# Kernel tuning notes

Hardware: AMD Instinct MI355X
Metric: run time of the kernel (lower is better)

Reference implementation:

```python
import jax, jax.numpy as jnp
import numpy as np

INPUT_SIZE = 300
HIDDEN_SIZE = 600
NUM_LAYERS = 2
B, T = 64, 512


def setup_inputs() -> dict:
    key = jax.random.key(0)
    ks = jax.random.split(key, 2 + 4 * NUM_LAYERS)
    scale = 1.0 / np.sqrt(HIDDEN_SIZE)
    inp = {
        "start_input": jax.random.normal(ks[0], (B, T, INPUT_SIZE), dtype=jnp.float32),
        "hidden_state": jax.random.normal(ks[1], (NUM_LAYERS, B, HIDDEN_SIZE), dtype=jnp.float32),
    }
    for l in range(NUM_LAYERS):
        in_dim = INPUT_SIZE if l == 0 else HIDDEN_SIZE
        k0, k1, k2, k3 = ks[2 + 4 * l: 6 + 4 * l]
        inp[f"W_ih{l}"] = jax.random.uniform(k0, (3 * HIDDEN_SIZE, in_dim), minval=-scale, maxval=scale, dtype=jnp.float32)
        inp[f"W_hh{l}"] = jax.random.uniform(k1, (3 * HIDDEN_SIZE, HIDDEN_SIZE), minval=-scale, maxval=scale, dtype=jnp.float32)
        inp[f"b_ih{l}"] = jax.random.uniform(k2, (3 * HIDDEN_SIZE,), minval=-scale, maxval=scale, dtype=jnp.float32)
        inp[f"b_hh{l}"] = jax.random.uniform(k3, (3 * HIDDEN_SIZE,), minval=-scale, maxval=scale, dtype=jnp.float32)
    return inp


def _gru_layer(x, h0, W_ih, W_hh, b_ih, b_hh):
    # x: [B,T,D], h0: [B,H]. PyTorch GRU gate order: r, z, n.
    H = HIDDEN_SIZE
    gi_all = jnp.einsum("btd,gd->btg", x, W_ih) + b_ih  # [B,T,3H], input-side GEMM batched over time

    def step(h, gi):
        gh = h @ W_hh.T + b_hh  # [B,3H]
        r = jax.nn.sigmoid(gi[:, :H] + gh[:, :H])
        z = jax.nn.sigmoid(gi[:, H:2 * H] + gh[:, H:2 * H])
        n = jnp.tanh(gi[:, 2 * H:] + r * gh[:, 2 * H:])
        h_new = (1.0 - z) * n + z * h
        return h_new, h_new

    h_last, out = jax.lax.scan(step, h0, jnp.swapaxes(gi_all, 0, 1))  # scan over T
    return jnp.swapaxes(out, 0, 1), h_last  # [B,T,H], [B,H]


def reference(start_input, hidden_state, W_ih0, W_hh0, b_ih0, b_hh0, W_ih1, W_hh1, b_ih1, b_hh1):
    params = [(W_ih0, W_hh0, b_ih0, b_hh0), (W_ih1, W_hh1, b_ih1, b_hh1)]
    x = start_input
    h_finals = []
    for l in range(NUM_LAYERS):
        x, h_last = _gru_layer(x, hidden_state[l], *params[l])
        h_finals.append(h_last)
    # judge=True path: restack of per-timestep slices is identity on r_out
    ret = x
    hidden_out = jnp.stack(h_finals, axis=0)  # [num_layers, B, H]
    return ret, hidden_out
```

## Files before the change

### kernel.cpp

```cpp
#include <hip/hip_runtime.h>

#define B    64
#define T    512
#define H    600
#define G3   1800
#define IN0  300
#define NBLK 150
#define NTHR 256
#define KPAD 1208

#define WC0_OFF 0
#define WC0_SZ  (900 * G3)
#define WC1_OFF (WC0_OFF + WC0_SZ)
#define WC1_SZ  (1200 * G3)
#define BC0_OFF (WC1_OFF + WC1_SZ)
#define BC1_OFF (BC0_OFF + H * 4)
#define HA_OFF  (BC1_OFF + H * 4)
#define HB_OFF  (HA_OFF + B * H)
#define BAR_OFF (HB_OFF + B * H + 64)

__device__ __forceinline__ void grid_barrier(int* __restrict__ cnt, int* __restrict__ gen) {
    __syncthreads();
    if (threadIdx.x == 0) {
        int g = __hip_atomic_load(gen, __ATOMIC_RELAXED, __HIP_MEMORY_SCOPE_AGENT);
        int arrived = __hip_atomic_fetch_add(cnt, 1, __ATOMIC_ACQ_REL, __HIP_MEMORY_SCOPE_AGENT);
        if (arrived == NBLK - 1) {
            __hip_atomic_store(cnt, 0, __ATOMIC_RELAXED, __HIP_MEMORY_SCOPE_AGENT);
            __hip_atomic_fetch_add(gen, 1, __ATOMIC_ACQ_REL, __HIP_MEMORY_SCOPE_AGENT);
        } else {
            while (__hip_atomic_load(gen, __ATOMIC_ACQUIRE, __HIP_MEMORY_SCOPE_AGENT) == g) {
                __builtin_amdgcn_s_sleep(1);
            }
        }
    }
    __syncthreads();
}

__global__ void init_bar(int* bar) { bar[0] = 0; bar[32] = 0; }

__global__ void build_wc(const float* __restrict__ Wih, const float* __restrict__ Whh,
                         float* __restrict__ WC, int in_dim, int ktot) {
    int idx = blockIdx.x * blockDim.x + threadIdx.x;
    if (idx >= ktot * G3) return;
    int k = idx / G3;
    int c = idx - k * G3;
    int j = c / 3;
    int g = c - j * 3;
    int grow = g * H + j;
    float v = (k < in_dim) ? Wih[grow * in_dim + k] : Whh[grow * H + (k - in_dim)];
    WC[idx] = v;
}

__global__ void build_bc(const float* __restrict__ bih0, const float* __restrict__ bhh0,
                         const float* __restrict__ bih1, const float* __restrict__ bhh1,
                         float* __restrict__ BC0, float* __restrict__ BC1) {
    int j = blockIdx.x * blockDim.x + threadIdx.x;
    if (j >= H) return;
    BC0[j * 4 + 0] = bih0[j] + bhh0[j];
    BC0[j * 4 + 1] = bih0[H + j] + bhh0[H + j];
    BC0[j * 4 + 2] = bih0[2 * H + j];
    BC0[j * 4 + 3] = bhh0[2 * H + j];
    BC1[j * 4 + 0] = bih1[j] + bhh1[j];
    BC1[j * 4 + 1] = bih1[H + j] + bhh1[H + j];
    BC1[j * 4 + 2] = bih1[2 * H + j];
    BC1[j * 4 + 3] = bhh1[2 * H + j];
}

template<int N4, int CH>
__device__ __forceinline__ void dot3f(const float4* __restrict__ ap,
                                      const float* __restrict__ wr,
                                      const float* __restrict__ wz,
                                      const float* __restrict__ wn,
                                      float& sr, float& sz, float& sn) {
    constexpr int NCH = N4 / CH;
    static_assert(N4 % CH == 0, "chunking");
    float4 A[CH], Bf[CH];
    #pragma unroll
    for (int i = 0; i < CH; ++i) A[i] = ap[i];
    #pragma unroll 1
    for (int c = 0; c < NCH; c += 2) {
        if (c + 1 < NCH) {
            const float4* p = ap + (c + 1) * CH;
            #pragma unroll
            for (int i = 0; i < CH; ++i) Bf[i] = p[i];
        }
        #pragma unroll
        for (int i = 0; i < CH; ++i) {
            const int k = (c * CH + i) * 4;
            float4 a = A[i];
            const float4 wR = *(const float4*)(wr + k);
            const float4 wZ = *(const float4*)(wz + k);
            const float4 wN = *(const float4*)(wn + k);
            sr += a.x * wR.x + a.y * wR.y + a.z * wR.z + a.w * wR.w;
            sz += a.x * wZ.x + a.y * wZ.y + a.z * wZ.z + a.w * wZ.w;
            sn += a.x * wN.x + a.y * wN.y + a.z * wN.z + a.w * wN.w;
        }
        if (c + 1 < NCH) {
            if (c + 2 < NCH) {
                const float4* p = ap + (c + 2) * CH;
                #pragma unroll
                for (int i = 0; i < CH; ++i) A[i] = p[i];
            }
            #pragma unroll
            for (int i = 0; i < CH; ++i) {
                const int k = ((c + 1) * CH + i) * 4;
                float4 a = Bf[i];
                const float4 wR = *(const float4*)(wr + k);
                const float4 wZ = *(const float4*)(wz + k);
                const float4 wN = *(const float4*)(wn + k);
                sr += a.x * wR.x + a.y * wR.y + a.z * wR.z + a.w * wR.w;
                sz += a.x * wZ.x + a.y * wZ.y + a.z * wZ.z + a.w * wZ.w;
                sn += a.x * wN.x + a.y * wN.y + a.z * wN.z + a.w * wN.w;
            }
        }
    }
}

template<int LAYER>
__device__ void gru_layer(const float* xsrc, const float* __restrict__ hid,
                          const float* __restrict__ WC, const float* __restrict__ BC,
                          float* __restrict__ hA, float* __restrict__ hB,
                          float* ret, float* __restrict__ outh,
                          float* Wl, int* cnt, int* gen) {
    constexpr int IN_DIM = LAYER ? H : IN0;
    constexpr int K = IN_DIM + H;
    const int tid = threadIdx.x;
    const int bb = tid >> 2;
    const int jj = tid & 3;
    const int j = blockIdx.x * 4 + jj;
    const int wcol0 = blockIdx.x * 12;

    for (int idx = tid; idx < 12 * K; idx += NTHR) {
        int k = idx / 12;
        int c = idx - k * 12;
        Wl[c * KPAD + k] = WC[(size_t)k * G3 + wcol0 + c];
    }
    {
        int g = blockIdx.x * NTHR + tid;
        hA[g] = hid[g];
    }
    grid_barrier(cnt, gen);

    float* hc = hA;
    float* hn = hB;
    const float bx  = BC[j * 4 + 0];
    const float by  = BC[j * 4 + 1];
    const float bgn = BC[j * 4 + 2];
    const float bhn = BC[j * 4 + 3];
    const float* wr = &Wl[(jj * 3 + 0) * KPAD];
    const float* wz = &Wl[(jj * 3 + 1) * KPAD];
    const float* wn = &Wl[(jj * 3 + 2) * KPAD];
    float hold = 0.0f;
    float hnv = 0.0f;

    for (int t = 0; t < T; ++t) {
        float sr = 0.f, sz = 0.f, sgn = 0.f, shn = 0.f;
        dot3f<IN_DIM / 4, 15>((const float4*)(xsrc + ((size_t)bb * T + t) * IN_DIM),
                              wr, wz, wn, sr, sz, sgn);
        dot3f<H / 4, 15>((const float4*)(hc + bb * H),
                         wr + IN_DIM, wz + IN_DIM, wn + IN_DIM, sr, sz, shn);
        float r = 1.f / (1.f + __expf(-(sr + bx)));
        float z = 1.f / (1.f + __expf(-(sz + by)));
        float n = tanhf(sgn + bgn + r * (shn + bhn));
        float hv = hc[bb * H + j];
        hnv = (1.f - z) * n + z * hv;
        hn[bb * H + j] = hnv;
        if (LAYER == 0) {
            ret[((size_t)bb * T + t) * H + j] = hnv;
        } else {
            if (t > 0) ret[((size_t)bb * T + (t - 1)) * H + j] = hold;
            hold = hnv;
        }
        grid_barrier(cnt, gen);
        float* tmp = hc; hc = hn; hn = tmp;
    }
    if (LAYER == 1) {
        ret[((size_t)bb * T + (T - 1)) * H + j] = hold;
    }
    outh[bb * H + j] = hnv;
    grid_barrier(cnt, gen);
}

__global__ void __launch_bounds__(NTHR, 1) gru_main(
    const float* x0, const float* __restrict__ hid,
    const float* __restrict__ WC0, const float* __restrict__ WC1,
    const float* __restrict__ BC0, const float* __restrict__ BC1,
    float* __restrict__ hA, float* __restrict__ hB,
    float* ret, float* __restrict__ outh, int* bar) {
    __shared__ __align__(16) float Wl[12 * KPAD];
    int* cnt = bar;
    int* gen = bar + 32;
    gru_layer<0>(x0, hid,          WC0, BC0, hA, hB, ret, outh,         Wl, cnt, gen);
    gru_layer<1>(ret, hid + B * H, WC1, BC1, hA, hB, ret, outh + B * H, Wl, cnt, gen);
}

extern "C" void kernel_launch(void* const* d_in, const int* in_sizes, int n_in,
                              void* d_out, int out_size, void* d_ws, size_t ws_size,
                              hipStream_t stream) {
    const float* x0   = (const float*)d_in[0];
    const float* hid  = (const float*)d_in[1];
    const float* Wih0 = (const float*)d_in[2];
    const float* Whh0 = (const float*)d_in[3];
    const float* bih0 = (const float*)d_in[4];
    const float* bhh0 = (const float*)d_in[5];
    const float* Wih1 = (const float*)d_in[6];
    const float* Whh1 = (const float*)d_in[7];
    const float* bih1 = (const float*)d_in[8];
    const float* bhh1 = (const float*)d_in[9];

    float* ws  = (float*)d_ws;
    float* WC0 = ws + WC0_OFF;
    float* WC1 = ws + WC1_OFF;
    float* BC0 = ws + BC0_OFF;
    float* BC1 = ws + BC1_OFF;
    float* hA  = ws + HA_OFF;
    float* hB  = ws + HB_OFF;
    int*   bar = (int*)(ws + BAR_OFF);

    float* ret  = (float*)d_out;
    float* outh = ret + (size_t)B * T * H;

    {
        int n0 = 900 * G3;
        build_wc<<<(n0 + 255) / 256, 256, 0, stream>>>(Wih0, Whh0, WC0, IN0, 900);
        int n1 = 1200 * G3;
        build_wc<<<(n1 + 255) / 256, 256, 0, stream>>>(Wih1, Whh1, WC1, H, 1200);
        build_bc<<<(H + 255) / 256, 256, 0, stream>>>(bih0, bhh0, bih1, bhh1, BC0, BC1);
        init_bar<<<1, 1, 0, stream>>>(bar);
    }

    gru_main<<<dim3(NBLK), dim3(NTHR), 0, stream>>>(
        x0, hid, WC0, WC1, BC0, BC1, hA, hB, ret, outh, bar);
}
```

Before: 28.52 ms.

## Replace generation grid barrier with monotonic counter and relaxed atomic hidden-state exchange

Swaps the count/generation grid barrier for a single monotonically increasing counter that each block bumps and spins on until it reaches a per-phase target. Most barriers use relaxed atomics only, and a heavier acquire/release barrier is kept at the layer transition. Hidden-state reads and writes become device-scope relaxed atomic loads and stores (64-bit loads in a new dot routine), so coherence is handled without acquire/release fences. This is meant to cut the per-timestep synchronisation latency, at the risk of memory-ordering bugs, especially for the layer-1 reads of layer-0 outputs written through plain stores.

```diff
diff --git a/kernel.cpp b/kernel.cpp
--- a/kernel.cpp
+++ b/kernel.cpp
@@ -19,24 +19,26 @@
 #define HB_OFF  (HA_OFF + B * H)
 #define BAR_OFF (HB_OFF + B * H + 64)
 
-__device__ __forceinline__ void grid_barrier(int* __restrict__ cnt, int* __restrict__ gen) {
+__device__ __forceinline__ void bar_fast(int* cnt, int target) {
     __syncthreads();
     if (threadIdx.x == 0) {
-        int g = __hip_atomic_load(gen, __ATOMIC_RELAXED, __HIP_MEMORY_SCOPE_AGENT);
-        int arrived = __hip_atomic_fetch_add(cnt, 1, __ATOMIC_ACQ_REL, __HIP_MEMORY_SCOPE_AGENT);
-        if (arrived == NBLK - 1) {
-            __hip_atomic_store(cnt, 0, __ATOMIC_RELAXED, __HIP_MEMORY_SCOPE_AGENT);
-            __hip_atomic_fetch_add(gen, 1, __ATOMIC_ACQ_REL, __HIP_MEMORY_SCOPE_AGENT);
-        } else {
-            while (__hip_atomic_load(gen, __ATOMIC_ACQUIRE, __HIP_MEMORY_SCOPE_AGENT) == g) {
-                __builtin_amdgcn_s_sleep(1);
-            }
-        }
-    }
-    __syncthreads();
-}
-
-__global__ void init_bar(int* bar) { bar[0] = 0; bar[32] = 0; }
+        __hip_atomic_fetch_add(cnt, 1, __ATOMIC_RELAXED, __HIP_MEMORY_SCOPE_AGENT);
+        while (__hip_atomic_load(cnt, __ATOMIC_RELAXED, __HIP_MEMORY_SCOPE_AGENT) < target)
+            __builtin_amdgcn_s_sleep(2);
+    }
+    __syncthreads();
+}
+__device__ __forceinline__ void bar_heavy(int* cnt, int target) {
+    __syncthreads();
+    if (threadIdx.x == 0) {
+        __hip_atomic_fetch_add(cnt, 1, __ATOMIC_ACQ_REL, __HIP_MEMORY_SCOPE_AGENT);
+        while (__hip_atomic_load(cnt, __ATOMIC_ACQUIRE, __HIP_MEMORY_SCOPE_AGENT) < target)
+            __builtin_amdgcn_s_sleep(2);
+    }
+    __syncthreads();
+}
+
+__global__ void init_bar(int* bar) { bar[0] = 0; }
 
 __global__ void build_wc(const float* __restrict__ Wih, const float* __restrict__ Whh,
                          float* __restrict__ WC, int in_dim, int ktot) {
@@ -116,12 +118,67 @@
     }
 }
 
+template<int NU, int CH>
+__device__ __forceinline__ void dot3h(const unsigned long long* hp,
+                                      const float* __restrict__ wr,
+                                      const float* __restrict__ wz,
+                                      const float* __restrict__ wn,
+                                      float& sr, float& sz, float& sn) {
+    constexpr int NCH = NU / CH;
+    static_assert(NU % CH == 0 && CH % 2 == 0 && NCH % 2 == 0, "chunking");
+    unsigned long long A[CH], Bu[CH];
+    #pragma unroll
+    for (int i = 0; i < CH; ++i)
+        A[i] = __hip_atomic_load(hp + i, __ATOMIC_RELAXED, __HIP_MEMORY_SCOPE_AGENT);
+    #pragma unroll 1
+    for (int c = 0; c < NCH; c += 2) {
+        {
+            const unsigned long long* p = hp + (c + 1) * CH;
+            #pragma unroll
+            for (int i = 0; i < CH; ++i)
+                Bu[i] = __hip_atomic_load(p + i, __ATOMIC_RELAXED, __HIP_MEMORY_SCOPE_AGENT);
+        }
+        #pragma unroll
+        for (int i = 0; i < CH; i += 2) {
+            const int k = (c * CH + i) * 2;
+            float2 a0 = __builtin_bit_cast(float2, A[i]);
+            float2 a1 = __builtin_bit_cast(float2, A[i + 1]);
+            const float4 wR = *(const float4*)(wr + k);
+            const float4 wZ = *(const float4*)(wz + k);
+            const float4 wN = *(const float4*)(wn + k);
+            sr += a0.x * wR.x + a0.y * wR.y + a1.x * wR.z + a1.y * wR.w;
+            sz += a0.x * wZ.x + a0.y * wZ.y + a1.x * wZ.z + a1.y * wZ.w;
+            sn += a0.x * wN.x + a0.y * wN.y + a1.x * wN.z + a1.y * wN.w;
+        }
+        {
+            if (c + 2 < NCH) {
+                const unsigned long long* p = hp + (c + 2) * CH;
+                #pragma unroll
+                for (int i = 0; i < CH; ++i)
+                    A[i] = __hip_atomic_load(p + i, __ATOMIC_RELAXED, __HIP_MEMORY_SCOPE_AGENT);
+            }
+            #pragma unroll
+            for (int i = 0; i < CH; i += 2) {
+                const int k = ((c + 1) * CH + i) * 2;
+                float2 a0 = __builtin_bit_cast(float2, Bu[i]);
+                float2 a1 = __builtin_bit_cast(float2, Bu[i + 1]);
+                const float4 wR = *(const float4*)(wr + k);
+                const float4 wZ = *(const float4*)(wz + k);
+                const float4 wN = *(const float4*)(wn + k);
+                sr += a0.x * wR.x + a0.y * wR.y + a1.x * wR.z + a1.y * wR.w;
+                sz += a0.x * wZ.x + a0.y * wZ.y + a1.x * wZ.z + a1.y * wZ.w;
+                sn += a0.x * wN.x + a0.y * wN.y + a1.x * wN.z + a1.y * wN.w;
+            }
+        }
+    }
+}
+
 template<int LAYER>
 __device__ void gru_layer(const float* xsrc, const float* __restrict__ hid,
                           const float* __restrict__ WC, const float* __restrict__ BC,
                           float* __restrict__ hA, float* __restrict__ hB,
                           float* ret, float* __restrict__ outh,
-                          float* Wl, int* cnt, int* gen) {
+                          float* Wl, int* cnt, int& btgt) {
     constexpr int IN_DIM = LAYER ? H : IN0;
     constexpr int K = IN_DIM + H;
     const int tid = threadIdx.x;
@@ -137,9 +194,10 @@
     }
     {
         int g = blockIdx.x * NTHR + tid;
-        hA[g] = hid[g];
-    }
-    grid_barrier(cnt, gen);
+        __hip_atomic_store(&hA[g], hid[g], __ATOMIC_RELAXED, __HIP_MEMORY_SCOPE_AGENT);
+    }
+    if (LAYER == 0) bar_fast(cnt, btgt); else bar_heavy(cnt, btgt);
+    btgt += NBLK;
 
     float* hc = hA;
     float* hn = hB;
@@ -157,28 +215,28 @@
         float sr = 0.f, sz = 0.f, sgn = 0.f, shn = 0.f;
         dot3f<IN_DIM / 4, 15>((const float4*)(xsrc + ((size_t)bb * T + t) * IN_DIM),
                               wr, wz, wn, sr, sz, sgn);
-        dot3f<H / 4, 15>((const float4*)(hc + bb * H),
+        dot3h<H / 2, 30>((const unsigned long long*)(hc + bb * H),
                          wr + IN_DIM, wz + IN_DIM, wn + IN_DIM, sr, sz, shn);
         float r = 1.f / (1.f + __expf(-(sr + bx)));
         float z = 1.f / (1.f + __expf(-(sz + by)));
         float n = tanhf(sgn + bgn + r * (shn + bhn));
-        float hv = hc[bb * H + j];
+        float hv = __hip_atomic_load(&hc[bb * H + j], __ATOMIC_RELAXED, __HIP_MEMORY_SCOPE_AGENT);
         hnv = (1.f - z) * n + z * hv;
-        hn[bb * H + j] = hnv;
+        __hip_atomic_store(&hn[bb * H + j], hnv, __ATOMIC_RELAXED, __HIP_MEMORY_SCOPE_AGENT);
         if (LAYER == 0) {
             ret[((size_t)bb * T + t) * H + j] = hnv;
         } else {
             if (t > 0) ret[((size_t)bb * T + (t - 1)) * H + j] = hold;
             hold = hnv;
         }
-        grid_barrier(cnt, gen);
+        bar_fast(cnt, btgt);
+        btgt += NBLK;
         float* tmp = hc; hc = hn; hn = tmp;
     }
     if (LAYER == 1) {
         ret[((size_t)bb * T + (T - 1)) * H + j] = hold;
     }
     outh[bb * H + j] = hnv;
-    grid_barrier(cnt, gen);
 }
 
 __global__ void __launch_bounds__(NTHR, 1) gru_main(
@@ -188,10 +246,9 @@
     float* __restrict__ hA, float* __restrict__ hB,
     float* ret, float* __restrict__ outh, int* bar) {
     __shared__ __align__(16) float Wl[12 * KPAD];
-    int* cnt = bar;
-    int* gen = bar + 32;
-    gru_layer<0>(x0, hid,          WC0, BC0, hA, hB, ret, outh,         Wl, cnt, gen);
-    gru_layer<1>(ret, hid + B * H, WC1, BC1, hA, hB, ret, outh + B * H, Wl, cnt, gen);
+    int btgt = NBLK;
+    gru_layer<0>(x0, hid,          WC0, BC0, hA, hB, ret, outh,         Wl, bar, btgt);
+    gru_layer<1>(ret, hid + B * H, WC1, BC1, hA, hB, ret, outh + B * H, Wl, bar, btgt);
 }
 
 extern "C" void kernel_launch(void* const* d_in, const int* in_sizes, int n_in,
```

After: 34.05 ms. 19.4% more time.
